# Kernel tuning notes

Measured on AMD Instinct MI355X. Metric: run time of the kernel, lower is better.

The kernel has to match this reference:

```python
import jax, jax.numpy as jnp
import numpy as np

B, S, D_IN, D_OUT = 8, 2048, 4096, 4096
RANK, N_ADAPTERS = 16, 8


def setup_inputs() -> dict:
    key = jax.random.key(0)
    k = jax.random.split(key, 6)
    x = jax.random.normal(k[0], (B, S, D_IN), dtype=jnp.float32)
    W = jax.random.normal(k[1], (D_OUT, D_IN), dtype=jnp.float32) * 0.02
    bias = jax.random.normal(k[2], (D_OUT,), dtype=jnp.float32) * 0.02
    lora_a = jax.random.normal(k[3], (N_ADAPTERS, RANK, D_IN), dtype=jnp.float32) * 0.02
    lora_b = jax.random.normal(k[4], (N_ADAPTERS, D_OUT, RANK), dtype=jnp.float32) * 0.02
    adapter_indices = jax.random.randint(k[5], (B,), 0, N_ADAPTERS, dtype=jnp.int64)
    return {"x": x, "W": W, "bias": bias, "lora_a": lora_a,
            "lora_b": lora_b, "adapter_indices": adapter_indices}


def reference(x, W, bias, lora_a, lora_b, adapter_indices):
    # Base linear: y = x @ W.T + bias
    base = jnp.einsum('bsi,oi->bso', x, W) + bias
    # Per-batch-element adapter gather (adapter index is shared across the seq dim)
    a = lora_a[adapter_indices]            # [B, r, D_in]
    b = lora_b[adapter_indices]            # [B, D_out, r]
    inter = jnp.einsum('bsi,bri->bsr', x, a)      # x_group @ a_i.T
    lora_out = jnp.einsum('bsr,bor->bso', inter, b)  # intermediate @ b_i.T
    return base + lora_out
```

## Files before the change

kernel.cpp:

```cpp
#include <hip/hip_runtime.h>


#define S_DIM   2048
#define DIN     4096
#define DOUT    4096
#define RANK    16
#define M_DIM   16384
#define K_DIM   DIN
#define N_DIM   DOUT

typedef __attribute__((ext_vector_type(8))) short  short8;
typedef __attribute__((ext_vector_type(4))) float  floatx4;

__device__ __forceinline__ unsigned short f2bf(float f) {
  union { float f; unsigned int u; } v; v.f = f;
  return (unsigned short)((v.u + 0x7FFFu + ((v.u >> 16) & 1u)) >> 16);
}
__device__ __forceinline__ unsigned int pk2(float a, float b) {
  return (unsigned int)f2bf(a) | ((unsigned int)f2bf(b) << 16);
}

__device__ __forceinline__ int load_adapter(const int* __restrict__ p, int b) {
  bool i64 = (p[1] == 0) & (p[3] == 0) & (p[5] == 0) & (p[7] == 0);
  return i64 ? p[2 * b] : p[b];
}

__device__ __forceinline__ void async16(const unsigned short* g, unsigned short* s) {
  __builtin_amdgcn_global_load_lds(
      (const __attribute__((address_space(1))) void*)g,
      (__attribute__((address_space(3))) void*)s, 16, 0, 0);
}

__device__ __forceinline__ void pack16_pad(const float* __restrict__ src,
                                           unsigned short* dst) {
  float4 v0 = ((const float4*)src)[0], v1 = ((const float4*)src)[1],
         v2 = ((const float4*)src)[2], v3 = ((const float4*)src)[3];
  uint4 p0, p1;
  p0.x = pk2(v0.x, v0.y); p0.y = pk2(v0.z, v0.w);
  p0.z = pk2(v1.x, v1.y); p0.w = pk2(v1.z, v1.w);
  p1.x = pk2(v2.x, v2.y); p1.y = pk2(v2.z, v2.w);
  p1.z = pk2(v3.x, v3.y); p1.w = pk2(v3.z, v3.w);
  ((uint4*)dst)[0] = p0;
  ((uint4*)dst)[1] = p1;
  uint4 z = make_uint4(0u, 0u, 0u, 0u);
  ((uint4*)dst)[2] = z;
  ((uint4*)dst)[3] = z;
}

__global__ __launch_bounds__(256) void conv_w(const float* __restrict__ w,
                                              unsigned short* __restrict__ wbf) {
  size_t base = ((size_t)blockIdx.x * 256 + threadIdx.x) * 8;
  const float4* src = (const float4*)(w + base);
  float4 f0 = src[0], f1 = src[1];
  uint4 p;
  p.x = pk2(f0.x, f0.y); p.y = pk2(f0.z, f0.w);
  p.z = pk2(f1.x, f1.y); p.w = pk2(f1.z, f1.w);
  *(uint4*)(wbf + base) = p;
}

__global__ __launch_bounds__(256) void conv_x_inter(
    const float* __restrict__ x,
    const float* __restrict__ lora_a,
    const int* __restrict__ adapters,
    unsigned short* __restrict__ xbf,
    float* __restrict__ inter) {
  __shared__ float a_lds[RANK][256];
  const int tid  = threadIdx.x;
  const int row0 = blockIdx.x * 16;
  const int adapter = load_adapter(adapters, row0 >> 11);
  const float* abase = lora_a + (size_t)adapter * RANK * DIN;
  const int rrow = tid >> 4;
  const int g    = tid & 15;
  const float* xrow = x + (size_t)(row0 + rrow) * DIN;
  unsigned short* xbrow = xbf + (size_t)(row0 + rrow) * DIN;

  float acc[RANK];
#pragma unroll
  for (int r = 0; r < RANK; ++r) acc[r] = 0.f;

  for (int kc = 0; kc < DIN; kc += 256) {
    __syncthreads();
#pragma unroll
    for (int i = 0; i < 4; ++i) {
      int fl = i * 1024 + tid * 4;
      int r = fl >> 8, c = fl & 255;
      *(float4*)&a_lds[r][c] = *(const float4*)(abase + (size_t)r * DIN + kc + c);
    }
    __syncthreads();
    float4 xv[4];
#pragma unroll
    for (int i = 0; i < 4; ++i) {
      int c = g * 4 + i * 64;
      xv[i] = *(const float4*)(xrow + kc + c);
      uint2 pb; pb.x = pk2(xv[i].x, xv[i].y); pb.y = pk2(xv[i].z, xv[i].w);
      *(uint2*)(xbrow + kc + c) = pb;
    }
#pragma unroll
    for (int r = 0; r < RANK; ++r) {
      float s = acc[r];
#pragma unroll
      for (int i = 0; i < 4; ++i) {
        const float* ap = &a_lds[r][g * 4 + i * 64];
        s += xv[i].x * ap[0] + xv[i].y * ap[1] + xv[i].z * ap[2] + xv[i].w * ap[3];
      }
      acc[r] = s;
    }
  }
#pragma unroll
  for (int m = 1; m < 16; m <<= 1)
#pragma unroll
    for (int r = 0; r < RANK; ++r) acc[r] += __shfl_xor(acc[r], m, 64);
  if (g == 0) {
    float* ip = inter + (size_t)(row0 + rrow) * RANK;
    float4 o;
    o.x = acc[0];  o.y = acc[1];  o.z = acc[2];  o.w = acc[3];  ((float4*)ip)[0] = o;
    o.x = acc[4];  o.y = acc[5];  o.z = acc[6];  o.w = acc[7];  ((float4*)ip)[1] = o;
    o.x = acc[8];  o.y = acc[9];  o.z = acc[10]; o.w = acc[11]; ((float4*)ip)[2] = o;
    o.x = acc[12]; o.y = acc[13]; o.z = acc[14]; o.w = acc[15]; ((float4*)ip)[3] = o;
  }
}

__global__ __launch_bounds__(256, 2) void gemm_lora(
    const unsigned short* __restrict__ A,
    const unsigned short* __restrict__ Bw,
    const float* __restrict__ bias,
    const float* __restrict__ inter,
    const float* __restrict__ lora_b,
    const int* __restrict__ adapters,
    float* __restrict__ out) {
  __shared__ unsigned short As[128 * 32];
  __shared__ unsigned short Bs[128 * 32];
  const int tid = threadIdx.x;
  const int wave = tid >> 6, lane = tid & 63;
  const int wm = wave >> 1, wn = wave & 1;
  const int row0 = blockIdx.y * 128, col0 = blockIdx.x * 128;

  const int lrow = lane >> 2, lcol = (lane & 3) * 8;
  const unsigned short* ag = A  + (size_t)(row0 + wave * 32 + lrow) * K_DIM + lcol;
  const unsigned short* bg = Bw + (size_t)(col0 + wave * 32 + lrow) * K_DIM + lcol;
  unsigned short* asd = As + wave * 1024;
  unsigned short* bsd = Bs + wave * 1024;

  const int fr = lane & 15, fq = lane >> 4;
  const unsigned short* afp = As + ((wm * 64 + fr) * 32 + fq * 8);
  const unsigned short* bfp = Bs + ((wn * 64 + fr) * 32 + fq * 8);

  floatx4 acc[4][4] = {};

  for (int k0 = 0; k0 < K_DIM; k0 += 32) {
    __syncthreads();
    async16(ag + k0, asd);
    async16(ag + k0 + (size_t)16 * K_DIM, asd + 512);
    async16(bg + k0, bsd);
    async16(bg + k0 + (size_t)16 * K_DIM, bsd + 512);
    __syncthreads();
    short8 af[4], bf[4];
#pragma unroll
    for (int i = 0; i < 4; ++i) af[i] = *(const short8*)(afp + i * 512);
#pragma unroll
    for (int i = 0; i < 4; ++i) bf[i] = *(const short8*)(bfp + i * 512);
#pragma unroll
    for (int mt = 0; mt < 4; ++mt)
#pragma unroll
      for (int nt = 0; nt < 4; ++nt)
        acc[mt][nt] = __builtin_amdgcn_mfma_f32_16x16x32_bf16(
            af[mt], bf[nt], acc[mt][nt], 0, 0, 0);
  }

  const int adapter = load_adapter(adapters, row0 >> 11);
  __syncthreads();
  if (tid < 128) {
    pack16_pad(inter + (size_t)(row0 + tid) * RANK, As + tid * 32);
  } else {
    int c = tid - 128;
    pack16_pad(lora_b + ((size_t)adapter * N_DIM + (col0 + c)) * RANK, Bs + c * 32);
  }
  __syncthreads();
  {
    short8 af[4], bf[4];
#pragma unroll
    for (int i = 0; i < 4; ++i) af[i] = *(const short8*)(afp + i * 512);
#pragma unroll
    for (int i = 0; i < 4; ++i) bf[i] = *(const short8*)(bfp + i * 512);
#pragma unroll
    for (int mt = 0; mt < 4; ++mt)
#pragma unroll
      for (int nt = 0; nt < 4; ++nt)
        acc[mt][nt] = __builtin_amdgcn_mfma_f32_16x16x32_bf16(
            af[mt], bf[nt], acc[mt][nt], 0, 0, 0);
  }

#pragma unroll
  for (int nt = 0; nt < 4; ++nt) {
    int col = col0 + wn * 64 + nt * 16 + fr;
    float bv = bias[col];
#pragma unroll
    for (int mt = 0; mt < 4; ++mt) {
      int row = row0 + wm * 64 + mt * 16 + fq * 4;
      float* op = out + (size_t)row * N_DIM + col;
#pragma unroll
      for (int j = 0; j < 4; ++j)
        op[(size_t)j * N_DIM] = acc[mt][nt][j] + bv;
    }
  }
}

extern "C" void kernel_launch(void* const* d_in, const int* in_sizes, int n_in,
                              void* d_out, int out_size, void* d_ws, size_t ws_size,
                              hipStream_t stream) {
  const float* x      = (const float*)d_in[0];
  const float* W      = (const float*)d_in[1];
  const float* bias   = (const float*)d_in[2];
  const float* lora_a = (const float*)d_in[3];
  const float* lora_b = (const float*)d_in[4];
  const int*   aidx   = (const int*)d_in[5];
  float* out = (float*)d_out;

  const size_t xbf_bytes = (size_t)M_DIM * DIN * 2;
  const size_t wbf_bytes = (size_t)N_DIM * DIN * 2;
  unsigned short* xbf = (unsigned short*)d_ws;
  unsigned short* wbf = (unsigned short*)((char*)d_ws + xbf_bytes);
  float* inter = (float*)((char*)d_ws + xbf_bytes + wbf_bytes);

  conv_w<<<dim3((size_t)N_DIM * DIN / (256 * 8)), dim3(256), 0, stream>>>(W, wbf);
  conv_x_inter<<<dim3(M_DIM / 16), dim3(256), 0, stream>>>(x, lora_a, aidx, xbf, inter);
  gemm_lora<<<dim3(N_DIM / 128, M_DIM / 128), dim3(256), 0, stream>>>(
      xbf, wbf, bias, inter, lora_b, aidx, out);
}
```

Before: 1.132 ms.

## Compute LoRA intermediate with MFMA in the x-conversion kernel

Replaces the scalar FP32 dot-product loop (LDS-staged lora_a, 16 accumulators per thread, shuffle reduction) with a bf16 MFMA 16x16x32 per 32-wide K chunk. Each of the four waves takes a quarter of K, and the partial results are summed through LDS. This removes heavy VALU and LDS work from a kernel that is mostly bound by memory traffic, so it can run at the rate of the x read and bf16 write. The trade-off is that the x·A product is now rounded to bf16 before accumulation, and lora_a is read with a strided per-lane pattern.

Measured after the change: 1.123 ms. About the same (-0.8%).

```diff
diff --git a/kernel.cpp b/kernel.cpp
--- a/kernel.cpp
+++ b/kernel.cpp
@@ -58,65 +58,48 @@
   *(uint4*)(wbf + base) = p;
 }
 
-__global__ __launch_bounds__(256) void conv_x_inter(
+__global__ __launch_bounds__(256) void inter_conv_x(
     const float* __restrict__ x,
     const float* __restrict__ lora_a,
     const int* __restrict__ adapters,
     unsigned short* __restrict__ xbf,
     float* __restrict__ inter) {
-  __shared__ float a_lds[RANK][256];
-  const int tid  = threadIdx.x;
+  __shared__ floatx4 red[4][64];
+  const int tid = threadIdx.x, wave = tid >> 6, lane = tid & 63;
+  const int fr = lane & 15, fq = lane >> 4;
   const int row0 = blockIdx.x * 16;
   const int adapter = load_adapter(adapters, row0 >> 11);
-  const float* abase = lora_a + (size_t)adapter * RANK * DIN;
-  const int rrow = tid >> 4;
-  const int g    = tid & 15;
-  const float* xrow = x + (size_t)(row0 + rrow) * DIN;
-  unsigned short* xbrow = xbf + (size_t)(row0 + rrow) * DIN;
-
-  float acc[RANK];
-#pragma unroll
-  for (int r = 0; r < RANK; ++r) acc[r] = 0.f;
-
-  for (int kc = 0; kc < DIN; kc += 256) {
-    __syncthreads();
-#pragma unroll
-    for (int i = 0; i < 4; ++i) {
-      int fl = i * 1024 + tid * 4;
-      int r = fl >> 8, c = fl & 255;
-      *(float4*)&a_lds[r][c] = *(const float4*)(abase + (size_t)r * DIN + kc + c);
-    }
-    __syncthreads();
-    float4 xv[4];
-#pragma unroll
-    for (int i = 0; i < 4; ++i) {
-      int c = g * 4 + i * 64;
-      xv[i] = *(const float4*)(xrow + kc + c);
-      uint2 pb; pb.x = pk2(xv[i].x, xv[i].y); pb.y = pk2(xv[i].z, xv[i].w);
-      *(uint2*)(xbrow + kc + c) = pb;
-    }
-#pragma unroll
-    for (int r = 0; r < RANK; ++r) {
-      float s = acc[r];
-#pragma unroll
-      for (int i = 0; i < 4; ++i) {
-        const float* ap = &a_lds[r][g * 4 + i * 64];
-        s += xv[i].x * ap[0] + xv[i].y * ap[1] + xv[i].z * ap[2] + xv[i].w * ap[3];
-      }
-      acc[r] = s;
-    }
-  }
-#pragma unroll
-  for (int m = 1; m < 16; m <<= 1)
-#pragma unroll
-    for (int r = 0; r < RANK; ++r) acc[r] += __shfl_xor(acc[r], m, 64);
-  if (g == 0) {
-    float* ip = inter + (size_t)(row0 + rrow) * RANK;
-    float4 o;
-    o.x = acc[0];  o.y = acc[1];  o.z = acc[2];  o.w = acc[3];  ((float4*)ip)[0] = o;
-    o.x = acc[4];  o.y = acc[5];  o.z = acc[6];  o.w = acc[7];  ((float4*)ip)[1] = o;
-    o.x = acc[8];  o.y = acc[9];  o.z = acc[10]; o.w = acc[11]; ((float4*)ip)[2] = o;
-    o.x = acc[12]; o.y = acc[13]; o.z = acc[14]; o.w = acc[15]; ((float4*)ip)[3] = o;
+
+  const float* xp = x + (size_t)(row0 + fr) * DIN;
+  unsigned short* xq = xbf + (size_t)(row0 + fr) * DIN;
+  const float* ap = lora_a + ((size_t)adapter * RANK + fr) * DIN;
+
+  floatx4 acc = {};
+  const int kbeg = wave * 1024, kend = kbeg + 1024;
+  for (int k0 = kbeg; k0 < kend; k0 += 32) {
+    const int k = k0 + fq * 8;
+    float4 a0 = *(const float4*)(xp + k);
+    float4 a1 = *(const float4*)(xp + k + 4);
+    uint4 apk;
+    apk.x = pk2(a0.x, a0.y); apk.y = pk2(a0.z, a0.w);
+    apk.z = pk2(a1.x, a1.y); apk.w = pk2(a1.z, a1.w);
+    *(uint4*)(xq + k) = apk;
+    float4 b0 = *(const float4*)(ap + k);
+    float4 b1 = *(const float4*)(ap + k + 4);
+    uint4 bpk;
+    bpk.x = pk2(b0.x, b0.y); bpk.y = pk2(b0.z, b0.w);
+    bpk.z = pk2(b1.x, b1.y); bpk.w = pk2(b1.z, b1.w);
+    short8 af = *(short8*)&apk;
+    short8 bf_ = *(short8*)&bpk;
+    acc = __builtin_amdgcn_mfma_f32_16x16x32_bf16(af, bf_, acc, 0, 0, 0);
+  }
+  red[wave][lane] = acc;
+  __syncthreads();
+  if (wave == 0) {
+    floatx4 s = red[0][lane] + red[1][lane] + red[2][lane] + red[3][lane];
+#pragma unroll
+    for (int j = 0; j < 4; ++j)
+      inter[(size_t)(row0 + fq * 4 + j) * RANK + fr] = s[j];
   }
 }
 
@@ -223,7 +206,7 @@
   float* inter = (float*)((char*)d_ws + xbf_bytes + wbf_bytes);
 
   conv_w<<<dim3((size_t)N_DIM * DIN / (256 * 8)), dim3(256), 0, stream>>>(W, wbf);
-  conv_x_inter<<<dim3(M_DIM / 16), dim3(256), 0, stream>>>(x, lora_a, aidx, xbf, inter);
+  inter_conv_x<<<dim3(M_DIM / 16), dim3(256), 0, stream>>>(x, lora_a, aidx, xbf, inter);
   gemm_lora<<<dim3(N_DIM / 128, M_DIM / 128), dim3(256), 0, stream>>>(
       xbf, wbf, bias, inter, lora_b, aidx, out);
 }
```
